# Performance work log

Measured on AMD Instinct MI355X. Metric: run time of the kernel, lower is better.

## Reference

```python
import jax, jax.numpy as jnp
import numpy as np

RES = 56        # input_resolution
WS = 7          # window_size
C = 128         # embedding_dim
H_HEADS = 4     # num_heads
HID = 512       # mlp hidden_dim


def layer_norm(x, g, b, eps=1e-5):
    mu = jnp.mean(x, axis=-1, keepdims=True)
    var = jnp.var(x, axis=-1, keepdims=True)
    return (x - mu) * jax.lax.rsqrt(var + eps) * g + b


def window_partition(x):
    # [B, H, W, C] -> [B*nW, WS*WS, C]
    B = x.shape[0]
    n = RES // WS
    x = x.reshape(B, n, WS, n, WS, C)
    x = x.transpose(0, 1, 3, 2, 4, 5)  # B, n, n, WS, WS, C
    return x.reshape(B * n * n, WS * WS, C)


def window_reverse(x, B):
    # [B*nW, WS*WS, C] -> [B, H, W, C]
    n = RES // WS
    x = x.reshape(B, n, n, WS, WS, C)
    x = x.transpose(0, 1, 3, 2, 4, 5)
    return x.reshape(B, RES, RES, C)


def setup_inputs() -> dict:
    key = jax.random.key(0)
    ks = jax.random.split(key, 8)
    s = lambda fan: 1.0 / np.sqrt(fan)
    return {
        "x": jax.random.normal(ks[0], (32, RES, RES, C), jnp.float32),
        "ln1_g": jnp.ones((C,), jnp.float32),
        "ln1_b": jnp.zeros((C,), jnp.float32),
        "qkv_w": jax.random.normal(ks[1], (C, 3 * C), jnp.float32) * s(C),
        "qkv_b": jnp.zeros((3 * C,), jnp.float32),
        "proj_w": jax.random.normal(ks[2], (C, C), jnp.float32) * s(C),
        "proj_b": jnp.zeros((C,), jnp.float32),
        "ln2_g": jnp.ones((C,), jnp.float32),
        "ln2_b": jnp.zeros((C,), jnp.float32),
        "mlp_w1": jax.random.normal(ks[3], (C, HID), jnp.float32) * s(C),
        "mlp_b1": jnp.zeros((HID,), jnp.float32),
        "mlp_w2": jax.random.normal(ks[4], (HID, C), jnp.float32) * s(HID),
        "mlp_b2": jnp.zeros((C,), jnp.float32),
    }


def reference(x, ln1_g, ln1_b, qkv_w, qkv_b, proj_w, proj_b,
              ln2_g, ln2_b, mlp_w1, mlp_b1, mlp_w2, mlp_b2):
    B = x.shape[0]
    shortcut = x
    h = layer_norm(x, ln1_g, ln1_b)
    w = window_partition(h)                         # [Bw, T, C], T = WS*WS
    Bw, T, _ = w.shape
    hd = C // H_HEADS
    qkv = (w @ qkv_w + qkv_b).reshape(Bw, T, 3, H_HEADS, hd)
    q, k, v = jnp.moveaxis(qkv, 2, 0)               # each [Bw, T, H, hd]
    scale = 1.0 / jnp.sqrt(jnp.asarray(hd, w.dtype))
    attn = jnp.einsum('bqhd,bkhd->bhqk', q, k) * scale
    attn = jax.nn.softmax(attn, axis=-1)
    o = jnp.einsum('bhqk,bkhd->bqhd', attn, v).reshape(Bw, T, C)
    o = o @ proj_w + proj_b
    h = window_reverse(o, B)
    x = shortcut + h
    m = layer_norm(x, ln2_g, ln2_b)
    m = jax.nn.gelu(m @ mlp_w1 + mlp_b1, approximate=False) @ mlp_w2 + mlp_b2
    return x + m
```

## Files before the change

### kernel.cpp

```cpp
#include <hip/hip_runtime.h>

typedef unsigned short u16;
typedef unsigned int   u32;
typedef unsigned long long u64;
typedef __attribute__((ext_vector_type(8))) short short8;
typedef __attribute__((ext_vector_type(4))) float f32x4;

__device__ __forceinline__ float bf2f(u16 u)    { return __uint_as_float(((u32)u) << 16); }
__device__ __forceinline__ float bf2f_lo(u32 u) { return __uint_as_float(u << 16); }
__device__ __forceinline__ float bf2f_hi(u32 u) { return __uint_as_float(u & 0xffff0000u); }
__device__ __forceinline__ u16 f2bf(float f) {
  u32 u = __float_as_uint(f);
  return (u16)((u + 0x7fffu + ((u >> 16) & 1u)) >> 16);
}
__device__ __forceinline__ u32 pack2(float a, float b) {
  return (u32)f2bf(a) | ((u32)f2bf(b) << 16);
}

__device__ __forceinline__ int detect_f32(const void* x) {
  u32 wv = ((const u32*)x)[threadIdx.x & 63];
  int e = (wv >> 7) & 0xFF;
  u64 m = __ballot(e >= 110 && e <= 135);
  return (__popcll(m) < 32) ? 1 : 0;
}
__device__ __forceinline__ float ld1(const void* p, int i, int f32w) {
  return f32w ? ((const float*)p)[i] : bf2f(((const u16*)p)[i]);
}

__device__ __forceinline__ short8 ldfrag(const u16* p) {
  union { uint4 u4; short8 s8; } c;
  c.u4 = *(const uint4*)p;
  return c.s8;
}
#define MFMA(a, b, c) __builtin_amdgcn_mfma_f32_16x16x32_bf16(a, b, c, 0, 0, 0)


#define HS2  136
#define QS2  264
#define VTS   72
#define PSS   72
#define HCS  264

__global__ __launch_bounds__(256) void transpose_all(
    const void* __restrict__ Xdet,
    const void* __restrict__ w1, const void* __restrict__ w2,
    const void* __restrict__ qkvW, const void* __restrict__ projW,
    u16* __restrict__ W1t, u16* __restrict__ W2t,
    u16* __restrict__ qkvWt, u16* __restrict__ projWt)
{
  const int f32w = detect_f32(Xdet);
  int idx = blockIdx.x * 256 + threadIdx.x;
  if (idx < 32768) {
    int n = idx & 511, k2 = idx >> 9;
    u32 v = pack2(ld1(w1, (2 * k2) * 512 + n, f32w),
                  ld1(w1, (2 * k2 + 1) * 512 + n, f32w));
    ((u32*)W1t)[n * 64 + k2] = v;
  } else if (idx < 65536) {
    int j = idx - 32768;
    int n = j & 127, k2 = j >> 7;
    u32 v = pack2(ld1(w2, (2 * k2) * 128 + n, f32w),
                  ld1(w2, (2 * k2 + 1) * 128 + n, f32w));
    ((u32*)W2t)[n * 256 + k2] = v;
  } else if (idx < 90112) {
    int j = idx - 65536;
    int n = j % 384, k2 = j / 384;
    u32 v = pack2(ld1(qkvW, (2 * k2) * 384 + n, f32w),
                  ld1(qkvW, (2 * k2 + 1) * 384 + n, f32w));
    ((u32*)qkvWt)[n * 64 + k2] = v;
  } else if (idx < 98304) {
    int j = idx - 90112;
    int n = j & 127, k2 = j >> 7;
    u32 v = pack2(ld1(projW, (2 * k2) * 128 + n, f32w),
                  ld1(projW, (2 * k2 + 1) * 128 + n, f32w));
    ((u32*)projWt)[n * 64 + k2] = v;
  }
}

__global__ __launch_bounds__(512, 4) void swin_block_fused(
    const void* __restrict__ X,  const void* __restrict__ G1, const void* __restrict__ Bt1,
    const u16* __restrict__ qkvWt, const void* __restrict__ QB,
    const u16* __restrict__ projWt, const void* __restrict__ PB,
    const void* __restrict__ G2, const void* __restrict__ Bt2,
    const u16* __restrict__ W1t, const void* __restrict__ Bb1,
    const u16* __restrict__ W2t, const void* __restrict__ Bb2,
    void* __restrict__ X2)
{
  __shared__ __align__(16) char pool[73216];
  u16*   hbuf   = (u16*)pool;
  u16*   qsP    = (u16*)(pool + 17408);
  u16*   vT     = (u16*)(pool + 54272);
  u16*   n2     = (u16*)(pool + 17408);
  float* rmean  = (float*)(pool + 34816);
  float* rrstd  = (float*)(pool + 35072);
  u16*   hc     = (u16*)(pool + 35328);
  float* redsum = (float*)(pool + 69120);
  float* redsq  = (float*)(pool + 71168);

  const int tid = threadIdx.x, win = blockIdx.x;
  const int w = tid >> 6, lane = tid & 63;
  const int l15 = lane & 15, quad = lane >> 4;
  const int bb = win >> 6, wrem = win & 63;
  const int by = (wrem >> 3) * 7, bx = (wrem & 7) * 7;
  const int f32w = detect_f32(X);

  {
    u32* hz = (u32*)(hbuf + 49 * HS2);
    for (int i = tid; i < 15 * HS2 / 2; i += 512) hz[i] = 0;
  }
  for (int t = w; t < 49; t += 8) {
    int y = by + t / 7, x = bx + t % 7;
    size_t base = ((size_t)bb * 3136 + (size_t)y * 56 + x) * 128;
    float f0, f1;
    if (f32w) { float2 v = *(const float2*)((const float*)X + base + lane * 2); f0 = v.x; f1 = v.y; }
    else      { u32 u = *(const u32*)((const u16*)X + base + lane * 2); f0 = bf2f_lo(u); f1 = bf2f_hi(u); }
    float s = f0 + f1, q = f0 * f0 + f1 * f1;
    #pragma unroll
    for (int o = 32; o > 0; o >>= 1) { s += __shfl_xor(s, o, 64); q += __shfl_xor(q, o, 64); }
    float mean = s * (1.0f / 128.0f);
    float var  = q * (1.0f / 128.0f) - mean * mean;
    float rstd = rsqrtf(var + 1e-5f);
    float g0 = ld1(G1, lane * 2, f32w),  g1 = ld1(G1, lane * 2 + 1, f32w);
    float c0 = ld1(Bt1, lane * 2, f32w), c1 = ld1(Bt1, lane * 2 + 1, f32w);
    *(u32*)(hbuf + t * HS2 + lane * 2) =
        pack2((f0 - mean) * rstd * g0 + c0, (f1 - mean) * rstd * g1 + c1);
  }
  __syncthreads();

  {
    f32x4 acc[4][3];
    #pragma unroll
    for (int mt = 0; mt < 4; ++mt)
      #pragma unroll
      for (int nt = 0; nt < 3; ++nt) acc[mt][nt] = 0.0f;
    #pragma unroll
    for (int ks = 0; ks < 4; ++ks) {
      short8 a[4], b[3];
      #pragma unroll
      for (int mt = 0; mt < 4; ++mt)
        a[mt] = ldfrag(hbuf + (mt * 16 + l15) * HS2 + ks * 32 + quad * 8);
      #pragma unroll
      for (int nt = 0; nt < 3; ++nt)
        b[nt] = ldfrag(qkvWt + (size_t)(w * 48 + nt * 16 + l15) * 128 + ks * 32 + quad * 8);
      #pragma unroll
      for (int mt = 0; mt < 4; ++mt)
        #pragma unroll
        for (int nt = 0; nt < 3; ++nt)
          acc[mt][nt] = MFMA(a[mt], b[nt], acc[mt][nt]);
    }
    #pragma unroll
    for (int nt = 0; nt < 3; ++nt) {
      int col = w * 48 + nt * 16 + l15;
      float bias = ld1(QB, col, f32w);
      int isv = (w * 48 + nt * 16) >= 256;
      #pragma unroll
      for (int mt = 0; mt < 4; ++mt) {
        #pragma unroll
        for (int r = 0; r < 4; ++r) {
          int m = mt * 16 + quad * 4 + r;
          u16 val = f2bf(acc[mt][nt][r] + bias);
          if (isv) vT[(col - 256) * VTS + m] = val;
          else     qsP[m * QS2 + col] = val;
        }
      }
    }
  }
  __syncthreads();

  const int hd = w >> 1, mrow0 = (w & 1) * 32;
  float p[2][4][4];
  {
    f32x4 s[2][4];
    #pragma unroll
    for (int mt = 0; mt < 2; ++mt)
      #pragma unroll
      for (int nt = 0; nt < 4; ++nt) s[mt][nt] = 0.0f;
    short8 aQ[2], bK[4];
    #pragma unroll
    for (int mt = 0; mt < 2; ++mt)
      aQ[mt] = ldfrag(qsP + (mrow0 + mt * 16 + l15) * QS2 + hd * 32 + quad * 8);
    #pragma unroll
    for (int nt = 0; nt < 4; ++nt)
      bK[nt] = ldfrag(qsP + (nt * 16 + l15) * QS2 + 128 + hd * 32 + quad * 8);
    #pragma unroll
    for (int mt = 0; mt < 2; ++mt)
      #pragma unroll
      for (int nt = 0; nt < 4; ++nt)
        s[mt][nt] = MFMA(aQ[mt], bK[nt], s[mt][nt]);
    const float scale = 0.17677669529663687f;
    #pragma unroll
    for (int mt = 0; mt < 2; ++mt) {
      #pragma unroll
      for (int r = 0; r < 4; ++r) {
        float v[4];
        #pragma unroll
        for (int nt = 0; nt < 4; ++nt) {
          int col = nt * 16 + l15;
          v[nt] = (col < 49) ? s[mt][nt][r] * scale : -1e30f;
        }
        float mx = fmaxf(fmaxf(v[0], v[1]), fmaxf(v[2], v[3]));
        #pragma unroll
        for (int o = 1; o < 16; o <<= 1) mx = fmaxf(mx, __shfl_xor(mx, o, 64));
        float e[4], sum = 0.f;
        #pragma unroll
        for (int nt = 0; nt < 4; ++nt) {
          e[nt] = (v[nt] > -1e29f) ? __expf(v[nt] - mx) : 0.0f;
          sum += e[nt];
        }
        #pragma unroll
        for (int o = 1; o < 16; o <<= 1) sum += __shfl_xor(sum, o, 64);
        float inv = 1.0f / sum;
        #pragma unroll
        for (int nt = 0; nt < 4; ++nt) p[mt][nt][r] = e[nt] * inv;
      }
    }
  }
  __syncthreads();

  #pragma unroll
  for (int mt = 0; mt < 2; ++mt)
    #pragma unroll
    for (int r = 0; r < 4; ++r) {
      u16* rowp = qsP + hd * (64 * PSS) + (mrow0 + mt * 16 + quad * 4 + r) * PSS;
      #pragma unroll
      for (int nt = 0; nt < 4; ++nt)
        rowp[nt * 16 + l15] = f2bf(p[mt][nt][r]);
    }
  __syncthreads();

  {
    f32x4 o[2][2];
    #pragma unroll
    for (int mt = 0; mt < 2; ++mt) { o[mt][0] = 0.0f; o[mt][1] = 0.0f; }
    #pragma unroll
    for (int ks = 0; ks < 2; ++ks) {
      short8 pf[2], vv[2];
      #pragma unroll
      for (int mt = 0; mt < 2; ++mt)
        pf[mt] = ldfrag(qsP + hd * (64 * PSS) + (mrow0 + mt * 16 + l15) * PSS + ks * 32 + quad * 8);
      #pragma unroll
      for (int nt = 0; nt < 2; ++nt)
        vv[nt] = ldfrag(vT + (hd * 32 + nt * 16 + l15) * VTS + ks * 32 + quad * 8);
      #pragma unroll
      for (int mt = 0; mt < 2; ++mt)
        #pragma unroll
        for (int nt = 0; nt < 2; ++nt)
          o[mt][nt] = MFMA(pf[mt], vv[nt], o[mt][nt]);
    }
    #pragma unroll
    for (int mt = 0; mt < 2; ++mt)
      #pragma unroll
      for (int nt = 0; nt < 2; ++nt)
        #pragma unroll
        for (int r = 0; r < 4; ++r)
          hbuf[(mrow0 + mt * 16 + quad * 4 + r) * HS2 + hd * 32 + nt * 16 + l15] =
              f2bf(o[mt][nt][r]);
  }
  __syncthreads();

  const int col = w * 16 + l15;
  float pax2[4][4];
  {
    float xr[4][4];
    #pragma unroll
    for (int mt = 0; mt < 4; ++mt)
      #pragma unroll
      for (int r = 0; r < 4; ++r) {
        int m = mt * 16 + quad * 4 + r;
        float v = 0.0f;
        if (m < 49) {
          int y = by + m / 7, x = bx + m % 7;
          size_t base = ((size_t)bb * 3136 + (size_t)y * 56 + x) * 128 + col;
          v = f32w ? ((const float*)X)[base] : bf2f(((const u16*)X)[base]);
        }
        xr[mt][r] = v;
      }
    f32x4 pa[4];
    #pragma unroll
    for (int mt = 0; mt < 4; ++mt) pa[mt] = 0.0f;
    #pragma unroll
    for (int ks = 0; ks < 4; ++ks) {
      short8 a[4];
      #pragma unroll
      for (int mt = 0; mt < 4; ++mt)
        a[mt] = ldfrag(hbuf + (mt * 16 + l15) * HS2 + ks * 32 + quad * 8);
      short8 b = ldfrag(projWt + (size_t)(w * 16 + l15) * 128 + ks * 32 + quad * 8);
      #pragma unroll
      for (int mt = 0; mt < 4; ++mt)
        pa[mt] = MFMA(a[mt], b, pa[mt]);
    }
    float bias = ld1(PB, col, f32w);
    #pragma unroll
    for (int mt = 0; mt < 4; ++mt) {
      #pragma unroll
      for (int r = 0; r < 4; ++r) {
        int m = mt * 16 + quad * 4 + r;
        pax2[mt][r] = (m < 49) ? (pa[mt][r] + bias + xr[mt][r]) : 0.0f;
      }
    }
  }

  #pragma unroll
  for (int mt = 0; mt < 4; ++mt)
    #pragma unroll
    for (int r = 0; r < 4; ++r) {
      float s = pax2[mt][r], q = s * s;
      #pragma unroll
      for (int o = 1; o < 16; o <<= 1) { s += __shfl_xor(s, o, 64); q += __shfl_xor(q, o, 64); }
      if (l15 == 0) {
        int m = mt * 16 + quad * 4 + r;
        redsum[m * 8 + w] = s;
        redsq [m * 8 + w] = q;
      }
    }
  __syncthreads();

  {
    int row = w * 8 + (lane >> 3), j = lane & 7;
    float s = redsum[row * 8 + j], q = redsq[row * 8 + j];
    #pragma unroll
    for (int o = 1; o < 8; o <<= 1) { s += __shfl_xor(s, o, 64); q += __shfl_xor(q, o, 64); }
    if (j == 0) {
      float mean = s * (1.0f / 128.0f);
      float var  = q * (1.0f / 128.0f) - mean * mean;
      rmean[row] = mean;
      rrstd[row] = rsqrtf(var + 1e-5f);
    }
  }
  __syncthreads();

  {
    float gcol = ld1(G2, col, f32w), bcol = ld1(Bt2, col, f32w);
    #pragma unroll
    for (int mt = 0; mt < 4; ++mt)
      #pragma unroll
      for (int r = 0; r < 4; ++r) {
        int m = mt * 16 + quad * 4 + r;
        float nv = (pax2[mt][r] - rmean[m]) * rrstd[m] * gcol + bcol;
        n2[m * HS2 + col] = f2bf(nv);
      }
  }
  __syncthreads();

  f32x4 oacc[4];
  #pragma unroll
  for (int mt = 0; mt < 4; ++mt) oacc[mt] = 0.0f;

  for (int ch = 0; ch < 2; ++ch) {
    f32x4 g1a[4][2];
    #pragma unroll
    for (int mt = 0; mt < 4; ++mt)
      #pragma unroll
      for (int nt = 0; nt < 2; ++nt) g1a[mt][nt] = 0.0f;
    #pragma unroll
    for (int ks = 0; ks < 4; ++ks) {
      short8 a[4], b[2];
      #pragma unroll
      for (int mt = 0; mt < 4; ++mt)
        a[mt] = ldfrag(n2 + (mt * 16 + l15) * HS2 + ks * 32 + quad * 8);
      #pragma unroll
      for (int nt = 0; nt < 2; ++nt)
        b[nt] = ldfrag(W1t + (size_t)(ch * 256 + w * 32 + nt * 16 + l15) * 128 + ks * 32 + quad * 8);
      #pragma unroll
      for (int mt = 0; mt < 4; ++mt)
        #pragma unroll
        for (int nt = 0; nt < 2; ++nt)
          g1a[mt][nt] = MFMA(a[mt], b[nt], g1a[mt][nt]);
    }
    #pragma unroll
    for (int nt = 0; nt < 2; ++nt) {
      int colg = ch * 256 + w * 32 + nt * 16 + l15;
      float bias1 = ld1(Bb1, colg, f32w);
      #pragma unroll
      for (int mt = 0; mt < 4; ++mt)
        #pragma unroll
        for (int r = 0; r < 4; ++r) {
          int m = mt * 16 + quad * 4 + r;
          float gl = 0.0f;
          if (m < 49) {
            float t2 = g1a[mt][nt][r] + bias1;
            gl = 0.5f * t2 * (1.0f + erff(t2 * 0.70710678118654752f));
          }
          hc[m * HCS + w * 32 + nt * 16 + l15] = f2bf(gl);
        }
    }
    __syncthreads();
    #pragma unroll
    for (int ks = 0; ks < 8; ++ks) {
      short8 a[4];
      #pragma unroll
      for (int mt = 0; mt < 4; ++mt)
        a[mt] = ldfrag(hc + (mt * 16 + l15) * HCS + ks * 32 + quad * 8);
      short8 b = ldfrag(W2t + (size_t)(w * 16 + l15) * 512 + ch * 256 + ks * 32 + quad * 8);
      #pragma unroll
      for (int mt = 0; mt < 4; ++mt)
        oacc[mt] = MFMA(a[mt], b, oacc[mt]);
    }
    __syncthreads();
  }

  {
    float bias2 = ld1(Bb2, col, f32w);
    #pragma unroll
    for (int mt = 0; mt < 4; ++mt) {
      #pragma unroll
      for (int r = 0; r < 4; ++r) {
        int m = mt * 16 + quad * 4 + r;
        if (m < 49) {
          int y = by + m / 7, x = bx + m % 7;
          size_t base = ((size_t)bb * 3136 + (size_t)y * 56 + x) * 128 + col;
          float v = oacc[mt][r] + bias2 + pax2[mt][r];
          if (f32w) ((float*)X2)[base] = v;
          else      ((u16*)X2)[base] = f2bf(v);
        }
      }
    }
  }
}

extern "C" void kernel_launch(void* const* d_in, const int* in_sizes, int n_in,
                              void* d_out, int out_size, void* d_ws, size_t ws_size,
                              hipStream_t stream)
{
  (void)in_sizes; (void)n_in; (void)out_size; (void)ws_size;
  const void* X = d_in[0];
  u16* W1t   = (u16*)d_ws;
  u16* W2t   = (u16*)((char*)d_ws + 131072);
  u16* qkvWt = (u16*)((char*)d_ws + 262144);
  u16* projWt= (u16*)((char*)d_ws + 360448);

  transpose_all<<<384, 256, 0, stream>>>(X, d_in[9], d_in[11], d_in[3], d_in[5],
                                         W1t, W2t, qkvWt, projWt);
  swin_block_fused<<<2048, 512, 0, stream>>>(X, d_in[1], d_in[2], qkvWt, d_in[4],
                                             projWt, d_in[6], d_in[7], d_in[8],
                                             W1t, d_in[10], W2t, d_in[12], d_out);
}
```

Before: 319.1 us.

## Shrink shared memory pool by aliasing buffers to raise occupancy

Cuts the fused kernel's LDS pool from about 72KB to 53KB. It does this by aliasing the LN output, the V transpose, the Q/K and P tiles, the attention output and the reduction buffers across phases, with an XOR-swizzled V layout to avoid bank conflicts. Extra __syncthreads barriers guard the reuse, and launch bounds are raised to 6 blocks per SM. The aim is more resident blocks to hide latency, at the cost of more barriers and possible register spills under the tighter bound.

Measured after the change: 398.2 us. 1.25x slower.

```diff
diff --git a/kernel.cpp b/kernel.cpp
--- a/kernel.cpp
+++ b/kernel.cpp
@@ -37,7 +37,6 @@
 
 #define HS2  136
 #define QS2  264
-#define VTS   72
 #define PSS   72
 #define HCS  264
 
@@ -76,7 +75,7 @@
   }
 }
 
-__global__ __launch_bounds__(512, 4) void swin_block_fused(
+__global__ __launch_bounds__(512, 6) void swin_block_fused(
     const void* __restrict__ X,  const void* __restrict__ G1, const void* __restrict__ Bt1,
     const u16* __restrict__ qkvWt, const void* __restrict__ QB,
     const u16* __restrict__ projWt, const void* __restrict__ PB,
@@ -85,16 +84,18 @@
     const u16* __restrict__ W2t, const void* __restrict__ Bb2,
     void* __restrict__ X2)
 {
-  __shared__ __align__(16) char pool[73216];
+  __shared__ __align__(16) char pool[54272];
   u16*   hbuf   = (u16*)pool;
-  u16*   qsP    = (u16*)(pool + 17408);
-  u16*   vT     = (u16*)(pool + 54272);
-  u16*   n2     = (u16*)(pool + 17408);
-  float* rmean  = (float*)(pool + 34816);
-  float* rrstd  = (float*)(pool + 35072);
-  u16*   hc     = (u16*)(pool + 35328);
-  float* redsum = (float*)(pool + 69120);
-  float* redsq  = (float*)(pool + 71168);
+  u16*   vTs    = (u16*)pool;
+  u16*   n2     = (u16*)pool;
+  u16*   qk     = (u16*)(pool + 17408);
+  u16*   Pb     = (u16*)(pool + 17408);
+  u16*   Obuf   = (u16*)(pool + 17408);
+  float* redsum = (float*)(pool + 17408);
+  float* redsq  = (float*)(pool + 19456);
+  u16*   hc     = (u16*)(pool + 17408);
+  float* rmean  = (float*)(pool + 51200);
+  float* rrstd  = (float*)(pool + 51456);
 
   const int tid = threadIdx.x, win = blockIdx.x;
   const int w = tid >> 6, lane = tid & 63;
@@ -126,40 +127,44 @@
   }
   __syncthreads();
 
-  {
-    f32x4 acc[4][3];
+  f32x4 acc[4][3];
+  #pragma unroll
+  for (int mt = 0; mt < 4; ++mt)
+    #pragma unroll
+    for (int nt = 0; nt < 3; ++nt) acc[mt][nt] = 0.0f;
+  #pragma unroll
+  for (int ks = 0; ks < 4; ++ks) {
+    short8 a[4], b[3];
     #pragma unroll
     for (int mt = 0; mt < 4; ++mt)
-      #pragma unroll
-      for (int nt = 0; nt < 3; ++nt) acc[mt][nt] = 0.0f;
-    #pragma unroll
-    for (int ks = 0; ks < 4; ++ks) {
-      short8 a[4], b[3];
-      #pragma unroll
-      for (int mt = 0; mt < 4; ++mt)
-        a[mt] = ldfrag(hbuf + (mt * 16 + l15) * HS2 + ks * 32 + quad * 8);
+      a[mt] = ldfrag(hbuf + (mt * 16 + l15) * HS2 + ks * 32 + quad * 8);
+    #pragma unroll
+    for (int nt = 0; nt < 3; ++nt)
+      b[nt] = ldfrag(qkvWt + (size_t)(w * 48 + nt * 16 + l15) * 128 + ks * 32 + quad * 8);
+    #pragma unroll
+    for (int mt = 0; mt < 4; ++mt)
       #pragma unroll
       for (int nt = 0; nt < 3; ++nt)
-        b[nt] = ldfrag(qkvWt + (size_t)(w * 48 + nt * 16 + l15) * 128 + ks * 32 + quad * 8);
-      #pragma unroll
-      for (int mt = 0; mt < 4; ++mt)
-        #pragma unroll
-        for (int nt = 0; nt < 3; ++nt)
-          acc[mt][nt] = MFMA(a[mt], b[nt], acc[mt][nt]);
-    }
-    #pragma unroll
-    for (int nt = 0; nt < 3; ++nt) {
-      int col = w * 48 + nt * 16 + l15;
-      float bias = ld1(QB, col, f32w);
-      int isv = (w * 48 + nt * 16) >= 256;
-      #pragma unroll
-      for (int mt = 0; mt < 4; ++mt) {
-        #pragma unroll
-        for (int r = 0; r < 4; ++r) {
-          int m = mt * 16 + quad * 4 + r;
-          u16 val = f2bf(acc[mt][nt][r] + bias);
-          if (isv) vT[(col - 256) * VTS + m] = val;
-          else     qsP[m * QS2 + col] = val;
+        acc[mt][nt] = MFMA(a[mt], b[nt], acc[mt][nt]);
+  }
+  __syncthreads();
+
+  #pragma unroll
+  for (int nt = 0; nt < 3; ++nt) {
+    int col = w * 48 + nt * 16 + l15;
+    float bias = ld1(QB, col, f32w);
+    int isv = (w * 48 + nt * 16) >= 256;
+    #pragma unroll
+    for (int mt = 0; mt < 4; ++mt) {
+      #pragma unroll
+      for (int r = 0; r < 4; ++r) {
+        int m = mt * 16 + quad * 4 + r;
+        u16 val = f2bf(acc[mt][nt][r] + bias);
+        if (isv) {
+          int vrow = col - 256;
+          vTs[vrow * 64 + (m ^ ((vrow & 7) << 3))] = val;
+        } else {
+          qk[m * QS2 + col] = val;
         }
       }
     }
@@ -177,10 +182,10 @@
     short8 aQ[2], bK[4];
     #pragma unroll
     for (int mt = 0; mt < 2; ++mt)
-      aQ[mt] = ldfrag(qsP + (mrow0 + mt * 16 + l15) * QS2 + hd * 32 + quad * 8);
+      aQ[mt] = ldfrag(qk + (mrow0 + mt * 16 + l15) * QS2 + hd * 32 + quad * 8);
     #pragma unroll
     for (int nt = 0; nt < 4; ++nt)
-      bK[nt] = ldfrag(qsP + (nt * 16 + l15) * QS2 + 128 + hd * 32 + quad * 8);
+      bK[nt] = ldfrag(qk + (nt * 16 + l15) * QS2 + 128 + hd * 32 + quad * 8);
     #pragma unroll
     for (int mt = 0; mt < 2; ++mt)
       #pragma unroll
@@ -220,41 +225,43 @@
   for (int mt = 0; mt < 2; ++mt)
     #pragma unroll
     for (int r = 0; r < 4; ++r) {
-      u16* rowp = qsP + hd * (64 * PSS) + (mrow0 + mt * 16 + quad * 4 + r) * PSS;
+      u16* rowp = Pb + hd * (64 * PSS) + (mrow0 + mt * 16 + quad * 4 + r) * PSS;
       #pragma unroll
       for (int nt = 0; nt < 4; ++nt)
         rowp[nt * 16 + l15] = f2bf(p[mt][nt][r]);
     }
   __syncthreads();
 
-  {
-    f32x4 o[2][2];
-    #pragma unroll
-    for (int mt = 0; mt < 2; ++mt) { o[mt][0] = 0.0f; o[mt][1] = 0.0f; }
-    #pragma unroll
-    for (int ks = 0; ks < 2; ++ks) {
-      short8 pf[2], vv[2];
-      #pragma unroll
-      for (int mt = 0; mt < 2; ++mt)
-        pf[mt] = ldfrag(qsP + hd * (64 * PSS) + (mrow0 + mt * 16 + l15) * PSS + ks * 32 + quad * 8);
+  f32x4 o2[2][2];
+  #pragma unroll
+  for (int mt = 0; mt < 2; ++mt) { o2[mt][0] = 0.0f; o2[mt][1] = 0.0f; }
+  #pragma unroll
+  for (int ks = 0; ks < 2; ++ks) {
+    short8 pf[2], vv[2];
+    #pragma unroll
+    for (int mt = 0; mt < 2; ++mt)
+      pf[mt] = ldfrag(Pb + hd * (64 * PSS) + (mrow0 + mt * 16 + l15) * PSS + ks * 32 + quad * 8);
+    #pragma unroll
+    for (int nt = 0; nt < 2; ++nt) {
+      int vrow = hd * 32 + nt * 16 + l15;
+      vv[nt] = ldfrag(vTs + vrow * 64 + ((ks * 32 + quad * 8) ^ ((l15 & 7) << 3)));
+    }
+    #pragma unroll
+    for (int mt = 0; mt < 2; ++mt)
       #pragma unroll
       for (int nt = 0; nt < 2; ++nt)
-        vv[nt] = ldfrag(vT + (hd * 32 + nt * 16 + l15) * VTS + ks * 32 + quad * 8);
-      #pragma unroll
-      for (int mt = 0; mt < 2; ++mt)
-        #pragma unroll
-        for (int nt = 0; nt < 2; ++nt)
-          o[mt][nt] = MFMA(pf[mt], vv[nt], o[mt][nt]);
-    }
-    #pragma unroll
-    for (int mt = 0; mt < 2; ++mt)
-      #pragma unroll
-      for (int nt = 0; nt < 2; ++nt)
-        #pragma unroll
-        for (int r = 0; r < 4; ++r)
-          hbuf[(mrow0 + mt * 16 + quad * 4 + r) * HS2 + hd * 32 + nt * 16 + l15] =
-              f2bf(o[mt][nt][r]);
-  }
+        o2[mt][nt] = MFMA(pf[mt], vv[nt], o2[mt][nt]);
+  }
+  __syncthreads();
+
+  #pragma unroll
+  for (int mt = 0; mt < 2; ++mt)
+    #pragma unroll
+    for (int nt = 0; nt < 2; ++nt)
+      #pragma unroll
+      for (int r = 0; r < 4; ++r)
+        Obuf[(mrow0 + mt * 16 + quad * 4 + r) * HS2 + hd * 32 + nt * 16 + l15] =
+            f2bf(o2[mt][nt][r]);
   __syncthreads();
 
   const int col = w * 16 + l15;
@@ -282,7 +289,7 @@
       short8 a[4];
       #pragma unroll
       for (int mt = 0; mt < 4; ++mt)
-        a[mt] = ldfrag(hbuf + (mt * 16 + l15) * HS2 + ks * 32 + quad * 8);
+        a[mt] = ldfrag(Obuf + (mt * 16 + l15) * HS2 + ks * 32 + quad * 8);
       short8 b = ldfrag(projWt + (size_t)(w * 16 + l15) * 128 + ks * 32 + quad * 8);
       #pragma unroll
       for (int mt = 0; mt < 4; ++mt)
@@ -298,6 +305,7 @@
       }
     }
   }
+  __syncthreads();
 
   #pragma unroll
   for (int mt = 0; mt < 4; ++mt)
```
